# Kernel tuning notes

Hardware: AMD Instinct MI355X
Metric: run time of the kernel (lower is better)

## Reference

```python
import jax, jax.numpy as jnp
import numpy as np
import math

B, S, DIM = 2, 2048, 1024
N_HEADS, N_KV = 16, 4
HD = DIM // N_HEADS          # 64
N_REP = N_HEADS // N_KV      # 4
ROPE_THETA = 5000.0


def _rope_tables(seqlen, head_dim, theta):
    freqs = 1.0 / (theta ** (np.arange(0, head_dim, 2, dtype=np.float32) / head_dim))
    angles = np.outer(np.arange(seqlen, dtype=np.float32), freqs)  # [S, HD/2]
    return jnp.asarray(np.cos(angles)), jnp.asarray(np.sin(angles))


def setup_inputs() -> dict:
    key = jax.random.key(0)
    ks = jax.random.split(key, 6)
    x = jax.random.normal(ks[0], (B, S, DIM), dtype=jnp.float32)
    cos, sin = _rope_tables(S, HD, ROPE_THETA)
    # additive causal mask: 0 on/below diagonal, -inf above
    mask = jnp.where(jnp.tril(jnp.ones((S, S), dtype=bool)), 0.0, -jnp.inf).astype(jnp.float32)
    wq = jax.random.normal(ks[1], (DIM, N_HEADS * HD), dtype=jnp.float32) * 0.02
    wk = jax.random.normal(ks[2], (DIM, N_KV * HD), dtype=jnp.float32) * 0.02
    wv = jax.random.normal(ks[3], (DIM, N_KV * HD), dtype=jnp.float32) * 0.02
    wo = jax.random.normal(ks[4], (N_HEADS * HD, DIM), dtype=jnp.float32) * 0.02
    return {"x": x, "cos": cos, "sin": sin, "mask": mask,
            "wq": wq, "wk": wk, "wv": wv, "wo": wo}


def _apply_rope(t, cos, sin):
    # t: [B, S, H, HD]; even/odd interleaved pairs form complex numbers
    te, to = t[..., 0::2], t[..., 1::2]               # [B,S,H,HD/2]
    c = cos[None, :, None, :]
    s = sin[None, :, None, :]
    re = te * c - to * s
    im = te * s + to * c
    return jnp.stack([re, im], axis=-1).reshape(t.shape)  # re-interleave


def reference(x, cos, sin, mask, wq, wk, wv, wo):
    bsz, seqlen, _ = x.shape
    q = (x @ wq).reshape(bsz, seqlen, N_HEADS, HD)
    k = (x @ wk).reshape(bsz, seqlen, N_KV, HD)
    v = (x @ wv).reshape(bsz, seqlen, N_KV, HD)
    q = _apply_rope(q, cos, sin)
    k = _apply_rope(k, cos, sin)
    # GQA: group query heads as [kv_head g, rep r] instead of repeating K/V
    qg = q.reshape(bsz, seqlen, N_KV, N_REP, HD)
    scores = jnp.einsum('bsgrd,btgd->bgrst', qg, k) / math.sqrt(HD)  # [B,G,R,S,S]
    scores = scores + mask[None, None, None, :, :]
    p = jax.nn.softmax(scores, axis=-1)
    out = jnp.einsum('bgrst,btgd->bsgrd', p, v)       # [B,S,G,R,HD]
    out = out.reshape(bsz, seqlen, N_HEADS * HD)
    return out @ wo
```

## Files before the change

kernel.cpp:

```cpp
#include <hip/hip_runtime.h>
#include <math.h>

#define S_LEN 2048
#define B_SZ 2

typedef __bf16 bf16_8 __attribute__((ext_vector_type(8)));
typedef float  f32_4  __attribute__((ext_vector_type(4)));

__device__ __forceinline__ unsigned short ftob(float f) {
  union { __bf16 h; unsigned short u; } cv;
  cv.h = (__bf16)f;
  return cv.u;
}

__device__ __forceinline__ void gll16(const unsigned short* g, unsigned short* l) {
  __builtin_amdgcn_global_load_lds(
      (const __attribute__((address_space(1))) unsigned int*)g,
      (__attribute__((address_space(3))) unsigned int*)l, 16, 0, 0);
}

#define QSCALE (0.125f * 1.44269504f)


__device__ __forceinline__ void tr_tile(const float* __restrict__ W,
                                        unsigned short* __restrict__ Wt,
                                        int N, int bx, int by, float (*T)[33])
{
  const int k0 = by * 32, n0 = bx * 32;
  const int r = threadIdx.x >> 3, c4 = (threadIdx.x & 7) * 4;
  const float4 v = *(const float4*)&W[(size_t)(k0 + r) * N + n0 + c4];
  T[r][c4 + 0] = v.x; T[r][c4 + 1] = v.y;
  T[r][c4 + 2] = v.z; T[r][c4 + 3] = v.w;
  __syncthreads();
  ushort4 o;
  o.x = ftob(T[c4 + 0][r]); o.y = ftob(T[c4 + 1][r]);
  o.z = ftob(T[c4 + 2][r]); o.w = ftob(T[c4 + 3][r]);
  *(ushort4*)&Wt[(size_t)(n0 + r) * 1024 + k0 + c4] = o;
}

__global__ __launch_bounds__(256) void prep(
    const float* __restrict__ x, const float* __restrict__ wq,
    const float* __restrict__ wk, const float* __restrict__ wv,
    const float* __restrict__ wo,
    unsigned short* __restrict__ xb, unsigned short* __restrict__ wqkvt,
    unsigned short* __restrict__ wot)
{
  __shared__ float T[32][33];
  const int idx = blockIdx.x;
  if (idx < 1024) {
    tr_tile(wq, wqkvt, 1024, idx & 31, idx >> 5, T);
  } else if (idx < 1280) {
    const int i = idx - 1024;
    tr_tile(wk, wqkvt + 1024 * 1024, 256, i & 7, i >> 3, T);
  } else if (idx < 1536) {
    const int i = idx - 1280;
    tr_tile(wv, wqkvt + 1280 * 1024, 256, i & 7, i >> 3, T);
  } else if (idx < 2560) {
    const int i = idx - 1536;
    tr_tile(wo, wot, 1024, i & 31, i >> 5, T);
  } else {
    const int i = idx - 2560;
#pragma unroll
    for (int j = 0; j < 4; ++j) {
      const int id = i * 1024 + (int)threadIdx.x + j * 256;
      const float4 v = ((const float4*)x)[id];
      ushort4 o;
      o.x = ftob(v.x); o.y = ftob(v.y); o.z = ftob(v.z); o.w = ftob(v.w);
      ((ushort4*)xb)[id] = o;
    }
  }
}

#define G64_KLOOP(A_, B_)                                                       \
  for (int k0 = 0; k0 < 1024; k0 += 32) {                                       \
    __syncthreads();                                                            \
    {                                                                           \
      const int r = tid >> 2, o8 = (tid & 3) * 8;                               \
      gll16(&A_[(size_t)(bm + r) * 1024 + k0 + o8], &sm[tid * 8]);              \
      gll16(&B_[(size_t)(bn0 * 128 + r) * 1024 + k0 + o8], &sm[2048 + tid * 8]);\
      gll16(&B_[(size_t)(bn0 * 128 + r + 64) * 1024 + k0 + o8],                 \
            &sm[2048 + (tid + 256) * 8]);                                       \
    }                                                                           \
    __syncthreads();                                                            \
    bf16_8 af[2], bf[4];                                                        \
    _Pragma("unroll")                                                           \
    for (int mt = 0; mt < 2; ++mt)                                              \
      af[mt] = *(const bf16_8*)&sm[(mh + mt * 16 + l16) * 32 + quad * 8];       \
    _Pragma("unroll")                                                           \
    for (int nt = 0; nt < 4; ++nt)                                              \
      bf[nt] = *(const bf16_8*)&sm[2048 + (nh + nt * 16 + l16) * 32 + quad * 8];\
    _Pragma("unroll")                                                           \
    for (int mt = 0; mt < 2; ++mt)                                              \
      _Pragma("unroll")                                                         \
      for (int nt = 0; nt < 4; ++nt)                                            \
        acc[mt][nt] = __builtin_amdgcn_mfma_f32_16x16x32_bf16(af[mt], bf[nt],   \
                                                              acc[mt][nt], 0, 0, 0); \
  }

__global__ __launch_bounds__(256, 3) void gemm_qkv(
    const unsigned short* __restrict__ A, const unsigned short* __restrict__ Bt,
    unsigned short* __restrict__ qb, unsigned short* __restrict__ Kimg,
    unsigned short* __restrict__ Vimg,
    const float* __restrict__ cosT, const float* __restrict__ sinT)
{
  __shared__ unsigned short sm[9216];
  const int bm = blockIdx.y * 64, bn0 = blockIdx.x;
  const int tid = threadIdx.x;
  const int w = tid >> 6, lane = tid & 63, l16 = lane & 15, quad = lane >> 4;
  const int mh = (w & 1) * 32, nh = (w >> 1) * 64;

  f32_4 acc[2][4];
#pragma unroll
  for (int mt = 0; mt < 2; ++mt)
#pragma unroll
    for (int nt = 0; nt < 4; ++nt) acc[mt][nt] = (f32_4){0.f, 0.f, 0.f, 0.f};

  G64_KLOOP(A, Bt);

  const int colbase = bn0 * 128;
  if (colbase < 1024) {
#pragma unroll
    for (int mt = 0; mt < 2; ++mt)
#pragma unroll
      for (int r = 0; r < 4; ++r) {
        const int row = bm + mh + mt * 16 + quad * 4 + r;
        const int s = row & (S_LEN - 1);
#pragma unroll
        for (int nt = 0; nt < 4; ++nt) {
          const int col = colbase + nh + nt * 16 + l16;
          float val = acc[mt][nt][r];
          const float pv = __shfl_xor(val, 1);
          const int fi = (col & 63) >> 1;
          const float cc = cosT[s * 32 + fi], ss = sinT[s * 32 + fi];
          val = (l16 & 1) ? fmaf(pv, ss, val * cc) : fmaf(val, cc, -(pv * ss));
          qb[(size_t)row * 1024 + col] = ftob(val * QSCALE);
        }
      }
  } else if (colbase < 1280) {
#pragma unroll
    for (int mt = 0; mt < 2; ++mt)
#pragma unroll
      for (int r = 0; r < 4; ++r) {
        const int row = bm + mh + mt * 16 + quad * 4 + r;
        const int s = row & (S_LEN - 1), bi = row >> 11;
        const int tile = s >> 6, key = s & 63;
#pragma unroll
        for (int nt = 0; nt < 4; ++nt) {
          const int col = colbase + nh + nt * 16 + l16;
          float val = acc[mt][nt][r];
          const float pv = __shfl_xor(val, 1);
          const int fi = (col & 63) >> 1;
          const float cc = cosT[s * 32 + fi], ss = sinT[s * 32 + fi];
          val = (l16 & 1) ? fmaf(pv, ss, val * cc) : fmaf(val, cc, -(pv * ss));
          const int gcol = col - 1024, g = gcol >> 6, d = gcol & 63;
          Kimg[(size_t)((bi * 4 + g) * 32 + tile) * 4096 + key * 64 +
               (((d >> 3) ^ (key & 7)) * 8) + (d & 7)] = ftob(val);
        }
      }
  } else {
    const int bi = bm >> 11, t0 = (bm & 2047) >> 6;
    const int gp = (bn0 - 10) * 2;
    __syncthreads();
    {
      unsigned short* Ts = sm + (w >> 1) * 4608;
#pragma unroll
      for (int mt = 0; mt < 2; ++mt)
#pragma unroll
        for (int nt = 0; nt < 4; ++nt) {
          const int keyb = mh + mt * 16 + quad * 4;
          const int d = nt * 16 + l16;
          ushort4 pk;
#pragma unroll
          for (int r = 0; r < 4; ++r) ((unsigned short*)&pk)[r] = ftob(acc[mt][nt][r]);
          *(ushort4*)&Ts[d * 72 + keyb] = pk;
        }
    }
    __syncthreads();
#pragma unroll
    for (int it = 0; it < 4; ++it) {
      const int c = tid + it * 256;
      const int img = c >> 9, cc = c & 511;
      const int d = cc >> 3, ch = cc & 7;
      const uint4 v = *(const uint4*)&sm[img * 4608 + d * 72 + ch * 8];
      *(uint4*)&Vimg[(size_t)((bi * 4 + gp + img) * 32 + t0) * 4096 + d * 64 +
                     ((ch ^ (d & 7)) * 8)] = v;
    }
  }
}

__global__ __launch_bounds__(256, 2) void gemm_wo(
    const unsigned short* __restrict__ A, const unsigned short* __restrict__ Bt,
    float* __restrict__ C)
{
  __shared__ unsigned short sm[6144];
  const int bm = blockIdx.y * 64, bn0 = blockIdx.x;
  const int tid = threadIdx.x;
  const int w = tid >> 6, lane = tid & 63, l16 = lane & 15, quad = lane >> 4;
  const int mh = (w & 1) * 32, nh = (w >> 1) * 64;

  f32_4 acc[2][4];
#pragma unroll
  for (int mt = 0; mt < 2; ++mt)
#pragma unroll
    for (int nt = 0; nt < 4; ++nt) acc[mt][nt] = (f32_4){0.f, 0.f, 0.f, 0.f};

  G64_KLOOP(A, Bt);

#pragma unroll
  for (int mt = 0; mt < 2; ++mt)
#pragma unroll
    for (int r = 0; r < 4; ++r) {
      const int row = bm + mh + mt * 16 + quad * 4 + r;
#pragma unroll
      for (int nt = 0; nt < 4; ++nt)
        C[(size_t)row * 1024 + bn0 * 128 + nh + nt * 16 + l16] = acc[mt][nt][r];
    }
}

__global__ __launch_bounds__(256) void flash_attn_v6(
    const unsigned short* __restrict__ Q, const unsigned short* __restrict__ Kimg,
    const unsigned short* __restrict__ Vimg, unsigned short* __restrict__ O)
{
  __shared__ unsigned short Ks[4096];
  __shared__ unsigned short Vs[4096];
  __shared__ unsigned short Ps[4][2048];
  const int id = blockIdx.x;
  const int gb = id & 7;
  const int g = gb & 3, b = gb >> 2;
  const int j = id >> 3;
  const int qc = (j < 32) ? (63 - j) : (j - 32);
  const int tid = threadIdx.x;
  const int w = tid >> 6, lane = tid & 63, l16 = lane & 15, quad = lane >> 4;
  const int h = g * 4 + w;
  const int qbase = qc * 32;
  const int swz = l16 & 7;
  unsigned short* ps = Ps[w];

  bf16_8 bq[2][2];
#pragma unroll
  for (int qf = 0; qf < 2; ++qf) {
    const unsigned short* qp =
        Q + ((size_t)(b * S_LEN + qbase + qf * 16 + l16)) * 1024 + h * 64;
    bq[qf][0] = *(const bf16_8*)(qp + quad * 8);
    bq[qf][1] = *(const bf16_8*)(qp + 32 + quad * 8);
  }

  f32_4 acc[2][4];
#pragma unroll
  for (int qf = 0; qf < 2; ++qf)
#pragma unroll
    for (int mt = 0; mt < 4; ++mt) acc[qf][mt] = (f32_4){0.f, 0.f, 0.f, 0.f};
  float l_part[2] = {0.f, 0.f};

  const unsigned short* kim = Kimg + (size_t)(gb * 32) * 4096;
  const unsigned short* vim = Vimg + (size_t)(gb * 32) * 4096;
  const int ntiles = (qc >> 1) + 1;

  uint4 r0, r1, r2, r3;
#define FA_LOAD(t)                                                              \
  do {                                                                          \
    const unsigned short* kp = kim + (size_t)(t) * 4096;                        \
    const unsigned short* vp = vim + (size_t)(t) * 4096;                        \
    r0 = *(const uint4*)(kp + tid * 8);                                         \
    r1 = *(const uint4*)(kp + (tid + 256) * 8);                                 \
    r2 = *(const uint4*)(vp + tid * 8);                                         \
    r3 = *(const uint4*)(vp + (tid + 256) * 8);                                 \
  } while (0)
#define FA_STORE()                                                              \
  do {                                                                          \
    *(uint4*)(Ks + tid * 8) = r0;                                               \
    *(uint4*)(Ks + (tid + 256) * 8) = r1;                                       \
    *(uint4*)(Vs + tid * 8) = r2;                                               \
    *(uint4*)(Vs + (tid + 256) * 8) = r3;                                       \
  } while (0)

  FA_LOAD(0);
  for (int tile = 0; tile < ntiles; ++tile) {
    __syncthreads();
    FA_STORE();
    if (tile + 1 < ntiles) FA_LOAD(tile + 1);
    __syncthreads();

    const bool diag = (tile == ntiles - 1);
#pragma unroll
    for (int mt = 0; mt < 4; ++mt) {
      const int krow = (mt * 16 + l16) * 64;
      const bf16_8 kf0 = *(const bf16_8*)&Ks[krow + (quad ^ swz) * 8];
      const bf16_8 kf1 = *(const bf16_8*)&Ks[krow + ((4 + quad) ^ swz) * 8];
#pragma unroll
      for (int qf = 0; qf < 2; ++qf) {
        f32_4 z = (f32_4){0.f, 0.f, 0.f, 0.f};
        z = __builtin_amdgcn_mfma_f32_16x16x32_bf16(kf0, bq[qf][0], z, 0, 0, 0);
        z = __builtin_amdgcn_mfma_f32_16x16x32_bf16(kf1, bq[qf][1], z, 0, 0, 0);
        ushort4 pk;
#pragma unroll
        for (int r = 0; r < 4; ++r) {
          float pv = __builtin_amdgcn_exp2f(z[r]);
          if (diag) {
            const int keyl = mt * 16 + quad * 4 + r;
            const int ql = (qc & 1) * 32 + qf * 16 + l16;
            pv = (keyl > ql) ? 0.f : pv;
          }
          l_part[qf] += pv;
          ((unsigned short*)&pk)[r] = ftob(pv);
        }
        *(ushort4*)&ps[(qf * 16 + l16) * 64 +
                       (((2 * mt + (quad >> 1)) ^ swz) * 8) + (quad & 1) * 4] = pk;
      }
    }
    bf16_8 pf[2][2];
#pragma unroll
    for (int qf = 0; qf < 2; ++qf) {
      const int prow = (qf * 16 + l16) * 64;
      pf[qf][0] = *(const bf16_8*)&ps[prow + ((quad ^ swz) * 8)];
      pf[qf][1] = *(const bf16_8*)&ps[prow + (((4 + quad) ^ swz) * 8)];
    }
#pragma unroll
    for (int mt = 0; mt < 4; ++mt) {
      const int vrow = (mt * 16 + l16) * 64;
      const bf16_8 vf0 = *(const bf16_8*)&Vs[vrow + (quad ^ swz) * 8];
      const bf16_8 vf1 = *(const bf16_8*)&Vs[vrow + ((4 + quad) ^ swz) * 8];
#pragma unroll
      for (int qf = 0; qf < 2; ++qf) {
        acc[qf][mt] = __builtin_amdgcn_mfma_f32_16x16x32_bf16(vf0, pf[qf][0], acc[qf][mt], 0, 0, 0);
        acc[qf][mt] = __builtin_amdgcn_mfma_f32_16x16x32_bf16(vf1, pf[qf][1], acc[qf][mt], 0, 0, 0);
      }
    }
  }

#pragma unroll
  for (int qf = 0; qf < 2; ++qf) {
    float l = l_part[qf];
    l += __shfl_xor(l, 16);
    l += __shfl_xor(l, 32);
    const float inv = 1.f / l;
    unsigned short* op =
        O + ((size_t)(b * S_LEN + qbase + qf * 16 + l16)) * 1024 + h * 64;
#pragma unroll
    for (int mt = 0; mt < 4; ++mt) {
      ushort4 ov;
#pragma unroll
      for (int r = 0; r < 4; ++r) ((unsigned short*)&ov)[r] = ftob(acc[qf][mt][r] * inv);
      *(ushort4*)&op[mt * 16 + quad * 4] = ov;
    }
  }
}

extern "C" void kernel_launch(void* const* d_in, const int* in_sizes, int n_in,
                              void* d_out, int out_size, void* d_ws, size_t ws_size,
                              hipStream_t stream)
{
  const float* x    = (const float*)d_in[0];
  const float* cosT = (const float*)d_in[1];
  const float* sinT = (const float*)d_in[2];
  const float* wq   = (const float*)d_in[4];
  const float* wk   = (const float*)d_in[5];
  const float* wv   = (const float*)d_in[6];
  const float* wo   = (const float*)d_in[7];
  float* out = (float*)d_out;

  char* ws = (char*)d_ws;
  const size_t MB = 1024 * 1024;
  unsigned short* xb    = (unsigned short*)(ws);
  unsigned short* qb    = (unsigned short*)(ws + 8 * MB);
  unsigned short* wqkvt = (unsigned short*)(ws + 16 * MB);
  unsigned short* Kimg  = (unsigned short*)(ws + 19 * MB);
  unsigned short* Vimg  = (unsigned short*)(ws + 21 * MB);
  unsigned short* wot   = (unsigned short*)(ws + 23 * MB);

  prep<<<3584, 256, 0, stream>>>(x, wq, wk, wv, wo, xb, wqkvt, wot);
  gemm_qkv<<<dim3(12, 64), 256, 0, stream>>>(xb, wqkvt, qb, Kimg, Vimg, cosT, sinT);
  flash_attn_v6<<<512, 256, 0, stream>>>(qb, Kimg, Vimg, qb);
  gemm_wo<<<dim3(8, 64), 256, 0, stream>>>(qb, wot, out);
}
```

Measured before the change: 172.9 us.

## Double-buffer GEMM K-loop with 64-wide stages and raise MFMA wave priority in attention

Both projection GEMMs switch to a double-buffered LDS pipeline. Each stage covers 64 of K, and the next stage's async global-to-LDS loads are issued before computing on the current buffer, which halves the barrier count and overlaps loads with MFMA. The attention kernel wraps its MFMA sections in s_setprio so that matrix-issuing waves are scheduled ahead of others. The cost is much more LDS per GEMM block (48 KB), which can reduce occupancy below the launch-bounds target.

```diff
diff --git a/kernel.cpp b/kernel.cpp
--- a/kernel.cpp
+++ b/kernel.cpp
@@ -71,30 +71,49 @@
   }
 }
 
-#define G64_KLOOP(A_, B_)                                                       \
-  for (int k0 = 0; k0 < 1024; k0 += 32) {                                       \
-    __syncthreads();                                                            \
-    {                                                                           \
-      const int r = tid >> 2, o8 = (tid & 3) * 8;                               \
-      gll16(&A_[(size_t)(bm + r) * 1024 + k0 + o8], &sm[tid * 8]);              \
-      gll16(&B_[(size_t)(bn0 * 128 + r) * 1024 + k0 + o8], &sm[2048 + tid * 8]);\
-      gll16(&B_[(size_t)(bn0 * 128 + r + 64) * 1024 + k0 + o8],                 \
-            &sm[2048 + (tid + 256) * 8]);                                       \
-    }                                                                           \
-    __syncthreads();                                                            \
-    bf16_8 af[2], bf[4];                                                        \
+#define G64DB_STAGE(A_, B_, bo_, k0_)                                           \
+  do {                                                                          \
+    const int r = tid >> 2, o8 = (tid & 3) * 8;                                 \
+    gll16(&A_[(size_t)(bm + r) * 1024 + (k0_) + o8], &sm[(bo_) + tid * 8]);     \
+    gll16(&A_[(size_t)(bm + r) * 1024 + (k0_) + 32 + o8],                       \
+          &sm[(bo_) + 2048 + tid * 8]);                                         \
+    gll16(&B_[(size_t)(bn0 * 128 + r) * 1024 + (k0_) + o8],                     \
+          &sm[(bo_) + 4096 + tid * 8]);                                         \
+    gll16(&B_[(size_t)(bn0 * 128 + r + 64) * 1024 + (k0_) + o8],                \
+          &sm[(bo_) + 6144 + tid * 8]);                                         \
+    gll16(&B_[(size_t)(bn0 * 128 + r) * 1024 + (k0_) + 32 + o8],                \
+          &sm[(bo_) + 8192 + tid * 8]);                                         \
+    gll16(&B_[(size_t)(bn0 * 128 + r + 64) * 1024 + (k0_) + 32 + o8],           \
+          &sm[(bo_) + 10240 + tid * 8]);                                        \
+  } while (0)
+
+#define G64DB_KLOOP(A_, B_)                                                     \
+  G64DB_STAGE(A_, B_, 0, 0);                                                    \
+  __syncthreads();                                                              \
+  for (int s = 0; s < 16; ++s) {                                                \
+    const int bo = (s & 1) * 12288;                                             \
+    if (s < 15) G64DB_STAGE(A_, B_, bo ^ 12288, (s + 1) * 64);                  \
+    bf16_8 af[2][2], bf[2][4];                                                  \
     _Pragma("unroll")                                                           \
-    for (int mt = 0; mt < 2; ++mt)                                              \
-      af[mt] = *(const bf16_8*)&sm[(mh + mt * 16 + l16) * 32 + quad * 8];       \
-    _Pragma("unroll")                                                           \
-    for (int nt = 0; nt < 4; ++nt)                                              \
-      bf[nt] = *(const bf16_8*)&sm[2048 + (nh + nt * 16 + l16) * 32 + quad * 8];\
-    _Pragma("unroll")                                                           \
-    for (int mt = 0; mt < 2; ++mt)                                              \
+    for (int ks = 0; ks < 2; ++ks) {                                            \
+      _Pragma("unroll")                                                         \
+      for (int mt = 0; mt < 2; ++mt)                                            \
+        af[ks][mt] = *(const bf16_8*)&sm[bo + ks * 2048 +                       \
+                                         (mh + mt * 16 + l16) * 32 + quad * 8]; \
       _Pragma("unroll")                                                         \
       for (int nt = 0; nt < 4; ++nt)                                            \
-        acc[mt][nt] = __builtin_amdgcn_mfma_f32_16x16x32_bf16(af[mt], bf[nt],   \
-                                                              acc[mt][nt], 0, 0, 0); \
+        bf[ks][nt] = *(const bf16_8*)&sm[bo + 4096 + ks * 4096 +                \
+                                         (nh + nt * 16 + l16) * 32 + quad * 8]; \
+    }                                                                           \
+    _Pragma("unroll")                                                           \
+    for (int ks = 0; ks < 2; ++ks)                                              \
+      _Pragma("unroll")                                                         \
+      for (int mt = 0; mt < 2; ++mt)                                            \
+        _Pragma("unroll")                                                       \
+        for (int nt = 0; nt < 4; ++nt)                                          \
+          acc[mt][nt] = __builtin_amdgcn_mfma_f32_16x16x32_bf16(                \
+              af[ks][mt], bf[ks][nt], acc[mt][nt], 0, 0, 0);                    \
+    __syncthreads();                                                            \
   }
 
 __global__ __launch_bounds__(256, 3) void gemm_qkv(
@@ -103,7 +122,7 @@
     unsigned short* __restrict__ Vimg,
     const float* __restrict__ cosT, const float* __restrict__ sinT)
 {
-  __shared__ unsigned short sm[9216];
+  __shared__ unsigned short sm[24576];
   const int bm = blockIdx.y * 64, bn0 = blockIdx.x;
   const int tid = threadIdx.x;
   const int w = tid >> 6, lane = tid & 63, l16 = lane & 15, quad = lane >> 4;
@@ -115,7 +134,7 @@
 #pragma unroll
     for (int nt = 0; nt < 4; ++nt) acc[mt][nt] = (f32_4){0.f, 0.f, 0.f, 0.f};
 
-  G64_KLOOP(A, Bt);
+  G64DB_KLOOP(A, Bt);
 
   const int colbase = bn0 * 128;
   if (colbase < 1024) {
@@ -192,7 +211,7 @@
     const unsigned short* __restrict__ A, const unsigned short* __restrict__ Bt,
     float* __restrict__ C)
 {
-  __shared__ unsigned short sm[6144];
+  __shared__ unsigned short sm[24576];
   const int bm = blockIdx.y * 64, bn0 = blockIdx.x;
   const int tid = threadIdx.x;
   const int w = tid >> 6, lane = tid & 63, l16 = lane & 15, quad = lane >> 4;
@@ -204,7 +223,7 @@
 #pragma unroll
     for (int nt = 0; nt < 4; ++nt) acc[mt][nt] = (f32_4){0.f, 0.f, 0.f, 0.f};
 
-  G64_KLOOP(A, Bt);
+  G64DB_KLOOP(A, Bt);
 
 #pragma unroll
   for (int mt = 0; mt < 2; ++mt)
@@ -217,7 +236,7 @@
     }
 }
 
-__global__ __launch_bounds__(256) void flash_attn_v6(
+__global__ __launch_bounds__(256) void flash_attn_v7(
     const unsigned short* __restrict__ Q, const unsigned short* __restrict__ Kimg,
     const unsigned short* __restrict__ Vimg, unsigned short* __restrict__ O)
 {
@@ -290,8 +309,10 @@
 #pragma unroll
       for (int qf = 0; qf < 2; ++qf) {
         f32_4 z = (f32_4){0.f, 0.f, 0.f, 0.f};
+        __builtin_amdgcn_s_setprio(1);
         z = __builtin_amdgcn_mfma_f32_16x16x32_bf16(kf0, bq[qf][0], z, 0, 0, 0);
         z = __builtin_amdgcn_mfma_f32_16x16x32_bf16(kf1, bq[qf][1], z, 0, 0, 0);
+        __builtin_amdgcn_s_setprio(0);
         ushort4 pk;
 #pragma unroll
         for (int r = 0; r < 4; ++r) {
@@ -315,6 +336,7 @@
       pf[qf][0] = *(const bf16_8*)&ps[prow + ((quad ^ swz) * 8)];
       pf[qf][1] = *(const bf16_8*)&ps[prow + (((4 + quad) ^ swz) * 8)];
     }
+    __builtin_amdgcn_s_setprio(1);
 #pragma unroll
     for (int mt = 0; mt < 4; ++mt) {
       const int vrow = (mt * 16 + l16) * 64;
@@ -326,6 +348,7 @@
         acc[qf][mt] = __builtin_amdgcn_mfma_f32_16x16x32_bf16(vf1, pf[qf][1], acc[qf][mt], 0, 0, 0);
       }
     }
+    __builtin_amdgcn_s_setprio(0);
   }
 
 #pragma unroll
@@ -370,6 +393,6 @@
 
   prep<<<3584, 256, 0, stream>>>(x, wq, wk, wv, wo, xb, wqkvt, wot);
   gemm_qkv<<<dim3(12, 64), 256, 0, stream>>>(xb, wqkvt, qb, Kimg, Vimg, cosT, sinT);
-  flash_attn_v6<<<512, 256, 0, stream>>>(qb, Kimg, Vimg, qb);
+  flash_attn_v7<<<512, 256, 0, stream>>>(qb, Kimg, Vimg, qb);
   gemm_wo<<<dim3(8, 64), 256, 0, stream>>>(qb, wot, out);
 }
```

Measured after the change: 168.4 us. 1.03x faster.
